# Kernel optimization log

Hardware: AMD Instinct MI355X
Metric: run time of the kernel (lower is better)

The kernel has to match this reference:

```python
import jax, jax.numpy as jnp
import numpy as np

THRESH = 0.3
PARTS = 6
D = 256
NHEAD = 8
DHEAD = 32
FF = 512
NLAYERS = 2
NUM_CLASSES = 396
EPS = 1e-5


def setup_inputs() -> dict:
    key = jax.random.key(0)
    ks = jax.random.split(key, 40)
    k = iter(ks)
    B, Q = 64, 300
    inp = {}
    inp["pred_logits"] = jax.random.normal(next(k), (B, Q, PARTS), jnp.float32)
    inp["hs"] = jax.random.normal(next(k), (B, Q, D), jnp.float32)
    for i, s in enumerate([96, 48, 24, 12]):
        inp[f"feat{i}"] = jax.random.normal(next(k), (B, D, s, s), jnp.float32)
    sc = 0.05
    inp["img_proj_w"] = sc * jax.random.normal(next(k), (4, D, D), jnp.float32)
    inp["img_proj_b"] = sc * jax.random.normal(next(k), (4, D), jnp.float32)
    inp["in_proj_w"] = sc * jax.random.normal(next(k), (NLAYERS, 3 * D, D), jnp.float32)
    inp["in_proj_b"] = sc * jax.random.normal(next(k), (NLAYERS, 3 * D), jnp.float32)
    inp["out_proj_w"] = sc * jax.random.normal(next(k), (NLAYERS, D, D), jnp.float32)
    inp["out_proj_b"] = sc * jax.random.normal(next(k), (NLAYERS, D), jnp.float32)
    inp["lin1_w"] = sc * jax.random.normal(next(k), (NLAYERS, FF, D), jnp.float32)
    inp["lin1_b"] = sc * jax.random.normal(next(k), (NLAYERS, FF), jnp.float32)
    inp["lin2_w"] = sc * jax.random.normal(next(k), (NLAYERS, D, FF), jnp.float32)
    inp["lin2_b"] = sc * jax.random.normal(next(k), (NLAYERS, D), jnp.float32)
    inp["ln1_w"] = jnp.ones((NLAYERS, D), jnp.float32)
    inp["ln1_b"] = jnp.zeros((NLAYERS, D), jnp.float32)
    inp["ln2_w"] = jnp.ones((NLAYERS, D), jnp.float32)
    inp["ln2_b"] = jnp.zeros((NLAYERS, D), jnp.float32)
    inp["cls1_w"] = sc * jax.random.normal(next(k), (512, D), jnp.float32)
    inp["cls1_b"] = sc * jax.random.normal(next(k), (512,), jnp.float32)
    inp["cls2_w"] = sc * jax.random.normal(next(k), (NUM_CLASSES, 512), jnp.float32)
    inp["cls2_b"] = sc * jax.random.normal(next(k), (NUM_CLASSES,), jnp.float32)
    return inp


def _layer_norm(x, w, b):
    m = jnp.mean(x, -1, keepdims=True)
    v = jnp.var(x, -1, keepdims=True)
    return (x - m) / jnp.sqrt(v + EPS) * w + b


def _forward(pred_logits, hs, feat0, feat1, feat2, feat3,
             img_proj_w, img_proj_b,
             in_proj_w, in_proj_b, out_proj_w, out_proj_b,
             lin1_w, lin1_b, lin2_w, lin2_b,
             ln1_w, ln1_b, ln2_w, ln2_b,
             cls1_w, cls1_b, cls2_w, cls2_b):
    B = hs.shape[0]
    # --- per-class masked mean pooling over queries (vectorized segment-mean) ---
    pred = jax.nn.sigmoid(pred_logits)                       # [B,Q,P]
    cmask = (pred > THRESH).astype(hs.dtype)                 # [B,Q,P]
    counts = cmask.sum(1)                                    # [B,P]
    csum = jnp.einsum("bqp,bqd->bpd", cmask, hs)             # [B,P,D]
    cmean = csum / jnp.maximum(counts, 1.0)[..., None]
    valid_c = counts > 0                                     # [B,P] bool
    any_valid = valid_c.any(1)                               # [B]
    # fallback: batches with no active class use hs[b, :1] in slot 0
    slot0 = jnp.where(any_valid[:, None], cmean[:, 0], hs[:, 0])
    cmean = cmean.at[:, 0].set(slot0)
    valid_c = valid_c.at[:, 0].set(valid_c[:, 0] | ~any_valid)
    # --- image tokens: global average pool + per-scale linear proj ---
    img_toks = jnp.stack([
        feat.mean((2, 3)) @ img_proj_w[i].T + img_proj_b[i]
        for i, feat in enumerate([feat0, feat1, feat2, feat3])
    ], axis=1)                                               # [B,4,D]
    tokens = jnp.concatenate([cmean, img_toks], 1)           # [B,L,D], L=PARTS+4
    valid = jnp.concatenate(
        [valid_c, jnp.ones((B, 4), bool)], 1)                # [B,L]
    NEG = jnp.asarray(-1e30, tokens.dtype)
    bias = jnp.where(valid, 0.0, NEG)[:, None, None, :]      # [B,1,1,L] key padding
    L = tokens.shape[1]
    x = tokens
    # --- 2-layer post-norm transformer encoder (eval mode, no dropout) ---
    for l in range(NLAYERS):
        qkv = x @ in_proj_w[l].T + in_proj_b[l]
        q, k_, v = jnp.split(qkv, 3, -1)
        q = q.reshape(B, L, NHEAD, DHEAD)
        k_ = k_.reshape(B, L, NHEAD, DHEAD)
        v = v.reshape(B, L, NHEAD, DHEAD)
        scores = jnp.einsum("bqhd,bkhd->bhqk", q, k_) / np.sqrt(DHEAD).astype(np.float32)
        attn = jax.nn.softmax(scores + bias, -1)
        ao = jnp.einsum("bhqk,bkhd->bqhd", attn, v).reshape(B, L, D)
        ao = ao @ out_proj_w[l].T + out_proj_b[l]
        x = _layer_norm(x + ao, ln1_w[l], ln1_b[l])
        ff = jax.nn.relu(x @ lin1_w[l].T + lin1_b[l]) @ lin2_w[l].T + lin2_b[l]
        x = _layer_norm(x + ff, ln2_w[l], ln2_b[l])
    # --- masked mean pool over valid tokens + classifier ---
    vf = valid.astype(x.dtype)
    lengths = jnp.maximum(vf.sum(1, keepdims=True), 1.0)
    cls_tok = (x * vf[..., None]).sum(1) / lengths           # [B,D]
    h = jax.nn.relu(cls_tok @ cls1_w.T + cls1_b)
    logits = h @ cls2_w.T + cls2_b                           # [B,NUM_CLASSES]
    return logits


def reference(pred_logits, hs, feat0, feat1, feat2, feat3,
              img_proj_w, img_proj_b,
              in_proj_w, in_proj_b, out_proj_w, out_proj_b,
              lin1_w, lin1_b, lin2_w, lin2_b,
              ln1_w, ln1_b, ln2_w, ln2_b,
              cls1_w, cls1_b, cls2_w, cls2_b):
    return _forward(pred_logits, hs, feat0, feat1, feat2, feat3,
                    img_proj_w, img_proj_b,
                    in_proj_w, in_proj_b, out_proj_w, out_proj_b,
                    lin1_w, lin1_b, lin2_w, lin2_b,
                    ln1_w, ln1_b, ln2_w, ln2_b,
                    cls1_w, cls1_b, cls2_w, cls2_b)
```

## Files before the change

kernel.cpp:

```cpp
#include <hip/hip_runtime.h>
#include <hip/hip_fp16.h>
#include <math.h>

#define NB 64
#define NQ 300
#define NP 6
#define ND 256
#define NF 512
#define NCL 396
#define NT 10

#define IPW_OFF 0
#define INW_OFF 262144
#define OW_OFF  655360
#define L1W_OFF 786432
#define L2W_OFF 1048576
#define C1W_OFF 1310720
#define C2W_OFF 1441792
#define TOTW    1644544
#define CONV_BLOCKS 803
#define POOL_ROWS 65536

typedef float f4 __attribute__((ext_vector_type(4)));

__device__ __forceinline__ float wred(float s) {
    #pragma unroll
    for (int o = 32; o; o >>= 1) s += __shfl_down(s, o, 64);
    return s;
}

__device__ __forceinline__ float dot8h(f4 wv, f4 xlo, f4 xhi) {
    const __half2* hp = reinterpret_cast<const __half2*>(&wv);
    float2 p0 = __half22float2(hp[0]);
    float2 p1 = __half22float2(hp[1]);
    float2 p2 = __half22float2(hp[2]);
    float2 p3 = __half22float2(hp[3]);
    return p0.x * xlo.x + p0.y * xlo.y + p1.x * xlo.z + p1.y * xlo.w
         + p2.x * xhi.x + p2.y * xhi.y + p3.x * xhi.z + p3.y * xhi.w;
}

__device__ __forceinline__ void qsync(int* flag, int tid) {
    __syncthreads();
    if (tid == 0) {
        __threadfence();
        __hip_atomic_fetch_add(flag, 1, __ATOMIC_ACQ_REL, __HIP_MEMORY_SCOPE_AGENT);
        while (__hip_atomic_load(flag, __ATOMIC_ACQUIRE, __HIP_MEMORY_SCOPE_AGENT) < 4)
            __builtin_amdgcn_s_sleep(2);
    }
    __syncthreads();
}

__global__ __launch_bounds__(256) void pool_cls_kernel(
    const float* __restrict__ pred, const float* __restrict__ hs,
    const float* __restrict__ f0, const float* __restrict__ f1,
    const float* __restrict__ f2, const float* __restrict__ f3,
    const float* __restrict__ ipw, const float* __restrict__ inw,
    const float* __restrict__ ow, const float* __restrict__ l1w,
    const float* __restrict__ l2w, const float* __restrict__ c1w,
    const float* __restrict__ c2w,
    float* __restrict__ pooled, float* __restrict__ tokG,
    float* __restrict__ biasW, __half* __restrict__ wH,
    int* __restrict__ flagW)
{
    const int bid = blockIdx.x;
    const int tid = threadIdx.x;
    __shared__ float shm[1824];

    if (bid < NB) {
        const int b = bid;
        if (tid < 16) flagW[b * 16 + tid] = 0;
        float* maskL = shm;
        float* countsL = shm + 1800;
        for (int i = tid; i < NQ * NP; i += 256) {
            float x = pred[(size_t)b * NQ * NP + i];
            float sg = 1.f / (1.f + expf(-x));
            maskL[i] = (sg > 0.3f) ? 1.f : 0.f;
        }
        __syncthreads();
        if (tid < NP) {
            float c = 0.f;
            for (int q = 0; q < NQ; q++) c += maskL[q * NP + tid];
            countsL[tid] = c;
        }
        __syncthreads();
        float acc[NP] = {0.f, 0.f, 0.f, 0.f, 0.f, 0.f};
        const float* hsb = hs + (size_t)b * NQ * ND + tid;
        for (int q = 0; q < NQ; q++) {
            float h = hsb[(size_t)q * ND];
            #pragma unroll
            for (int p = 0; p < NP; p++) acc[p] += maskL[q * NP + p] * h;
        }
        bool anyv = false;
        #pragma unroll
        for (int p = 0; p < NP; p++) anyv = anyv || (countsL[p] > 0.f);
        #pragma unroll
        for (int p = 0; p < NP; p++) {
            float cm = acc[p] / fmaxf(countsL[p], 1.f);
            if (p == 0 && !anyv) cm = hs[(size_t)b * NQ * ND + tid];
            tokG[(size_t)b * 2560 + p * ND + tid] = cm;
        }
        if (tid < 16) {
            float bv = 0.f;
            if (tid < NP) {
                bool v = countsL[tid] > 0.f;
                if (tid == 0 && !anyv) v = true;
                bv = v ? 0.f : -1e30f;
            }
            biasW[b * 16 + tid] = bv;
        }
        return;
    }

    if (bid >= NB + POOL_ROWS) {
        const int cid = bid - (NB + POOL_ROWS);
        size_t base = (size_t)cid * 2048 + (size_t)tid * 8;
        const float* src; size_t off;
        if      (base < INW_OFF) { src = ipw; off = IPW_OFF; }
        else if (base < OW_OFF)  { src = inw; off = INW_OFF; }
        else if (base < L1W_OFF) { src = ow;  off = OW_OFF;  }
        else if (base < L2W_OFF) { src = l1w; off = L1W_OFF; }
        else if (base < C1W_OFF) { src = l2w; off = L2W_OFF; }
        else if (base < C2W_OFF) { src = c1w; off = C1W_OFF; }
        else                     { src = c2w; off = C2W_OFF; }
        const f4* s4 = reinterpret_cast<const f4*>(src + (base - off));
        f4 a = s4[0], b2 = s4[1];
        union { __half2 h[4]; f4 v; } u;
        u.h[0] = __floats2half2_rn(a.x, a.y);
        u.h[1] = __floats2half2_rn(a.z, a.w);
        u.h[2] = __floats2half2_rn(b2.x, b2.y);
        u.h[3] = __floats2half2_rn(b2.z, b2.w);
        *reinterpret_cast<f4*>(wH + base) = u.v;
        return;
    }

    const int row = bid - NB;
    const int scale = row >> 14;
    const int rr = row & 16383;
    const int b = rr >> 8;
    const int d = rr & 255;
    const float* src;
    int n;
    switch (scale) {
        case 0: src = f0; n = 96 * 96; break;
        case 1: src = f1; n = 48 * 48; break;
        case 2: src = f2; n = 24 * 24; break;
        default: src = f3; n = 12 * 12; break;
    }
    const f4* p4 = reinterpret_cast<const f4*>(src + ((size_t)b * ND + d) * (size_t)n);
    int n4 = n >> 2;
    float s = 0.f;
    for (int i = tid; i < n4; i += 256) {
        f4 v = __builtin_nontemporal_load(&p4[i]);
        s += v.x + v.y + v.z + v.w;
    }
    s = wred(s);
    int wid = tid >> 6, lane = tid & 63;
    if (lane == 0) shm[wid] = s;
    __syncthreads();
    if (tid == 0) {
        float t = shm[0] + shm[1] + shm[2] + shm[3];
        pooled[((size_t)b * 4 + scale) * ND + d] = t / (float)n;
    }
}

__global__ __launch_bounds__(512) void xform_kernel(
    const float* __restrict__ pooled, float* tokG,
    const float* __restrict__ biasW, const __half* __restrict__ wH,
    const float* __restrict__ ipb, const float* __restrict__ inb,
    const float* __restrict__ ob, const float* __restrict__ l1b,
    const float* __restrict__ l2b,
    const float* __restrict__ n1w, const float* __restrict__ n1b,
    const float* __restrict__ n2w, const float* __restrict__ n2b,
    const float* __restrict__ c1b, const float* __restrict__ c2b,
    float* aoW, float* resW, float* h1W, float* hW,
    int* flagW, float* __restrict__ out)
{
    const int b  = blockIdx.x >> 2;
    const int qt = blockIdx.x & 3;
    const int tid = threadIdx.x;
    const int lane = tid & 63;
    const int wv = tid >> 6;
    int* flags = flagW + b * 16;

    __shared__ __align__(16) float xs[2560];
    __shared__ __align__(16) float loc[1920];
    __shared__ __align__(16) float buf[5120];
    __shared__ __align__(16) float part[5120];
    __shared__ float sc[224];
    __shared__ float stats[32];
    __shared__ float biasK[16];

    const f4* xs4 = reinterpret_cast<const f4*>(xs);
    const f4* buf4 = reinterpret_cast<const f4*>(buf);

    for (int i = tid; i < 1536; i += 512) xs[i] = tokG[(size_t)b * 2560 + i];
    for (int i = tid; i < 1024; i += 512) buf[i] = pooled[(size_t)b * 1024 + i];
    if (tid < 16) biasK[tid] = biasW[b * 16 + tid];
    __syncthreads();

    if (tid < 256) {
        const int i = tid >> 6, cl = tid & 63;
        const int c = qt * 64 + cl;
        const f4* w4 = reinterpret_cast<const f4*>(wH + IPW_OFF + ((size_t)(i * 256 + c)) * 256);
        float acc = 0.f;
        #pragma unroll 4
        for (int k8 = 0; k8 < 32; k8++)
            acc += dot8h(w4[k8], buf4[i * 64 + 2 * k8], buf4[i * 64 + 2 * k8 + 1]);
        tokG[(size_t)b * 2560 + (6 + i) * 256 + c] = acc + ipb[i * 256 + c];
    }
    qsync(&flags[0], tid);
    for (int i = tid + 1536; i < 2560; i += 512) xs[i] = tokG[(size_t)b * 2560 + i];
    __syncthreads();

    for (int l = 0; l < 2; l++) {
        if (tid < 384) {
            const int ks = tid / 192, cl = tid % 192;
            const int m = cl >> 6;
            const int gc = m * 256 + qt * 64 + (cl & 63);
            const f4* w4 = reinterpret_cast<const f4*>(wH + INW_OFF + ((size_t)l * 768 + gc) * 256 + ks * 128);
            float acc[NT];
            #pragma unroll
            for (int r = 0; r < NT; r++) acc[r] = 0.f;
            for (int k8 = 0; k8 < 16; k8++) {
                f4 wv4 = w4[k8];
                const int xi = ks * 32 + 2 * k8;
                #pragma unroll
                for (int r = 0; r < NT; r++)
                    acc[r] += dot8h(wv4, xs4[r * 64 + xi], xs4[r * 64 + xi + 1]);
            }
            #pragma unroll
            for (int r = 0; r < NT; r++) part[ks * 1920 + r * 192 + cl] = acc[r];
        }
        __syncthreads();
        for (int i = tid; i < 1920; i += 512) {
            int r = i / 192, cl = i - r * 192;
            int m = cl >> 6, gc = m * 256 + qt * 64 + (cl & 63);
            loc[i] = part[i] + part[1920 + i] + inb[l * 768 + gc];
        }
        __syncthreads();

        if (tid < 200) {
            int hl = tid / 100, rem = tid - 100 * hl;
            int qr = rem / 10, kr = rem - 10 * qr;
            const float* qp = &loc[qr * 192 + hl * 32];
            const float* kp = &loc[kr * 192 + 64 + hl * 32];
            float s = 0.f;
            #pragma unroll
            for (int d = 0; d < 32; d++) s += qp[d] * kp[d];
            sc[tid] = s * 0.17677669529663687f + biasK[kr];
        }
        __syncthreads();
        if (tid < 20) {
            float* row = &sc[tid * 10];
            float m = row[0];
            #pragma unroll
            for (int k = 1; k < 10; k++) m = fmaxf(m, row[k]);
            float ss = 0.f;
            #pragma unroll
            for (int k = 0; k < 10; k++) { float e = expf(row[k] - m); row[k] = e; ss += e; }
            float inv = 1.f / ss;
            #pragma unroll
            for (int k = 0; k < 10; k++) row[k] *= inv;
        }
        __syncthreads();

        for (int idx = tid; idx < 640; idx += 512) {
            int hl = idx / 320, rem = idx - 320 * hl;
            int r = rem >> 5, c = rem & 31;
            float s = 0.f;
            #pragma unroll
            for (int kr = 0; kr < 10; kr++)
                s += sc[hl * 100 + r * 10 + kr] * loc[kr * 192 + 128 + hl * 32 + c];
            aoW[(size_t)b * 2560 + r * 256 + qt * 64 + hl * 32 + c] = s;
        }
        qsync(&flags[1 + l * 4], tid);
        for (int i = tid; i < 2560; i += 512) buf[i] = aoW[(size_t)b * 2560 + i];
        __syncthreads();

        if (tid < 256) {
            const int ks = tid >> 6, cl = tid & 63;
            const int gc = qt * 64 + cl;
            const f4* w4 = reinterpret_cast<const f4*>(wH + OW_OFF + ((size_t)l * 256 + gc) * 256 + ks * 64);
            float acc[NT];
            #pragma unroll
            for (int r = 0; r < NT; r++) acc[r] = 0.f;
            for (int k8 = 0; k8 < 8; k8++) {
                f4 wv4 = w4[k8];
                const int xi = ks * 16 + 2 * k8;
                #pragma unroll
                for (int r = 0; r < NT; r++)
                    acc[r] += dot8h(wv4, buf4[r * 64 + xi], buf4[r * 64 + xi + 1]);
            }
            #pragma unroll
            for (int r = 0; r < NT; r++) part[ks * 640 + r * 64 + cl] = acc[r];
        }
        __syncthreads();
        for (int i = tid; i < 640; i += 512) {
            int r = i >> 6, cl = i & 63, gc = qt * 64 + cl;
            float v = part[i] + part[640 + i] + part[1280 + i] + part[1920 + i]
                    + ob[l * 256 + gc] + xs[r * 256 + gc];
            resW[(size_t)b * 2560 + r * 256 + gc] = v;
        }
        qsync(&flags[2 + l * 4], tid);
        for (int i = tid; i < 2560; i += 512) buf[i] = resW[(size_t)b * 2560 + i];
        __syncthreads();

        for (int r = wv; r < NT; r += 8) {
            float v0 = buf[r * 256 + lane], v1 = buf[r * 256 + 64 + lane];
            float v2 = buf[r * 256 + 128 + lane], v3 = buf[r * 256 + 192 + lane];
            float s = wred(v0 + v1 + v2 + v3);
            float q = wred(v0 * v0 + v1 * v1 + v2 * v2 + v3 * v3);
            if (lane == 0) {
                float m = s * (1.f / 256.f);
                stats[r] = m;
                stats[16 + r] = rsqrtf(fmaxf(q * (1.f / 256.f) - m * m, 0.f) + 1e-5f);
            }
        }
        __syncthreads();
        for (int i = tid; i < 2560; i += 512) {
            int r = i >> 8, c = i & 255;
            xs[i] = (buf[i] - stats[r]) * stats[16 + r] * n1w[l * 256 + c] + n1b[l * 256 + c];
        }
        __syncthreads();

        {
            const int ks = tid >> 7, cl = tid & 127;
            const int gc = qt * 128 + cl;
            const f4* w4 = reinterpret_cast<const f4*>(wH + L1W_OFF + ((size_t)l * 512 + gc) * 256 + ks * 64);
            float acc[NT];
            #pragma unroll
            for (int r = 0; r < NT; r++) acc[r] = 0.f;
            for (int k8 = 0; k8 < 8; k8++) {
                f4 wv4 = w4[k8];
                const int xi = ks * 16 + 2 * k8;
                #pragma unroll
                for (int r = 0; r < NT; r++)
                    acc[r] += dot8h(wv4, xs4[r * 64 + xi], xs4[r * 64 + xi + 1]);
            }
            __syncthreads();
            #pragma unroll
            for (int r = 0; r < NT; r++) buf[ks * 1280 + r * 128 + cl] = acc[r];
        }
        __syncthreads();
        for (int i = tid; i < 1280; i += 512) {
            int r = i >> 7, cl = i & 127, gc = qt * 128 + cl;
            float h = fmaxf(buf[i] + buf[1280 + i] + buf[2560 + i] + buf[3840 + i]
                          + l1b[l * 512 + gc], 0.f);
            h1W[(size_t)b * 5120 + r * 512 + gc] = h;
        }
        qsync(&flags[3 + l * 4], tid);
        for (int i = tid; i < 5120; i += 512) buf[i] = h1W[(size_t)b * 5120 + i];
        __syncthreads();

        {
            const int ks = tid >> 6, cl = tid & 63;
            const int gc = qt * 64 + cl;
            const f4* w4 = reinterpret_cast<const f4*>(wH + L2W_OFF + ((size_t)l * 256 + gc) * 512 + ks * 64);
            float acc[NT];
            #pragma unroll
            for (int r = 0; r < NT; r++) acc[r] = 0.f;
            for (int k8 = 0; k8 < 8; k8++) {
                f4 wv4 = w4[k8];
                const int xi = ks * 16 + 2 * k8;
                #pragma unroll
                for (int r = 0; r < NT; r++)
                    acc[r] += dot8h(wv4, buf4[r * 128 + xi], buf4[r * 128 + xi + 1]);
            }
            #pragma unroll
            for (int r = 0; r < NT; r++) part[ks * 640 + r * 64 + cl] = acc[r];
        }
        __syncthreads();
        for (int i = tid; i < 640; i += 512) {
            int r = i >> 6, cl = i & 63, gc = qt * 64 + cl;
            float v = part[i] + part[640 + i] + part[1280 + i] + part[1920 + i]
                    + part[2560 + i] + part[3200 + i] + part[3840 + i] + part[4480 + i]
                    + l2b[l * 256 + gc] + xs[r * 256 + gc];
            resW[(size_t)b * 2560 + r * 256 + gc] = v;
        }
        qsync(&flags[4 + l * 4], tid);
        for (int i = tid; i < 2560; i += 512) buf[i] = resW[(size_t)b * 2560 + i];
        __syncthreads();

        for (int r = wv; r < NT; r += 8) {
            float v0 = buf[r * 256 + lane], v1 = buf[r * 256 + 64 + lane];
            float v2 = buf[r * 256 + 128 + lane], v3 = buf[r * 256 + 192 + lane];
            float s = wred(v0 + v1 + v2 + v3);
            float q = wred(v0 * v0 + v1 * v1 + v2 * v2 + v3 * v3);
            if (lane == 0) {
                float m = s * (1.f / 256.f);
                stats[r] = m;
                stats[16 + r] = rsqrtf(fmaxf(q * (1.f / 256.f) - m * m, 0.f) + 1e-5f);
            }
        }
        __syncthreads();
        for (int i = tid; i < 2560; i += 512) {
            int r = i >> 8, c = i & 255;
            xs[i] = (buf[i] - stats[r]) * stats[16 + r] * n2w[l * 256 + c] + n2b[l * 256 + c];
        }
        __syncthreads();
    }

    if (tid < 256) {
        float len = 0.f, s = 0.f;
        #pragma unroll
        for (int r = 0; r < NT; r++) {
            float v = (biasK[r] == 0.f) ? 1.f : 0.f;
            len += v;
            s += v * xs[r * 256 + tid];
        }
        buf[tid] = s / fmaxf(len, 1.f);
    }
    __syncthreads();

    if (tid < 256) {
        const int ks = tid >> 7, cl = tid & 127;
        const int gc = qt * 128 + cl;
        const f4* w4 = reinterpret_cast<const f4*>(wH + C1W_OFF + (size_t)gc * 256 + ks * 128);
        float acc = 0.f;
        #pragma unroll 4
        for (int k8 = 0; k8 < 16; k8++)
            acc += dot8h(w4[k8], buf4[ks * 32 + 2 * k8], buf4[ks * 32 + 2 * k8 + 1]);
        part[ks * 128 + cl] = acc;
    }
    __syncthreads();
    if (tid < 128) {
        const int gc = qt * 128 + tid;
        hW[(size_t)b * 512 + gc] = fmaxf(part[tid] + part[128 + tid] + c1b[gc], 0.f);
    }
    qsync(&flags[9], tid);
    for (int i = tid; i < 512; i += 512) buf[i] = hW[(size_t)b * 512 + i];
    __syncthreads();

    if (tid < 99) {
        const int o = qt * 99 + tid;
        const f4* w4 = reinterpret_cast<const f4*>(wH + C2W_OFF + (size_t)o * 512);
        float acc = 0.f;
        #pragma unroll 4
        for (int k8 = 0; k8 < 64; k8++)
            acc += dot8h(w4[k8], buf4[2 * k8], buf4[2 * k8 + 1]);
        out[(size_t)b * NCL + o] = acc + c2b[o];
    }
}

extern "C" void kernel_launch(void* const* d_in, const int* in_sizes, int n_in,
                              void* d_out, int out_size, void* d_ws, size_t ws_size,
                              hipStream_t stream)
{
    const float* pred = (const float*)d_in[0];
    const float* hs   = (const float*)d_in[1];
    const float* f0   = (const float*)d_in[2];
    const float* f1   = (const float*)d_in[3];
    const float* f2   = (const float*)d_in[4];
    const float* f3   = (const float*)d_in[5];
    const float* ipw  = (const float*)d_in[6];
    const float* ipb  = (const float*)d_in[7];
    const float* inw  = (const float*)d_in[8];
    const float* inb  = (const float*)d_in[9];
    const float* ow   = (const float*)d_in[10];
    const float* ob   = (const float*)d_in[11];
    const float* l1w  = (const float*)d_in[12];
    const float* l1b  = (const float*)d_in[13];
    const float* l2w  = (const float*)d_in[14];
    const float* l2b  = (const float*)d_in[15];
    const float* ln1w = (const float*)d_in[16];
    const float* ln1b = (const float*)d_in[17];
    const float* ln2w = (const float*)d_in[18];
    const float* ln2b = (const float*)d_in[19];
    const float* c1w  = (const float*)d_in[20];
    const float* c1b  = (const float*)d_in[21];
    const float* c2w  = (const float*)d_in[22];
    const float* c2b  = (const float*)d_in[23];

    float* ws = (float*)d_ws;
    float* pooled = ws;
    float* tokG   = pooled + NB * 4 * ND;
    float* biasW  = tokG + NB * 2560;
    __half* wH    = (__half*)(biasW + 1024);
    float* aoW    = (float*)(wH + TOTW);
    float* resW   = aoW + NB * 2560;
    float* h1W    = resW + NB * 2560;
    float* hW     = h1W + NB * 5120;
    int*   flagW  = (int*)(hW + NB * 512);

    pool_cls_kernel<<<NB + POOL_ROWS + CONV_BLOCKS, 256, 0, stream>>>(
        pred, hs, f0, f1, f2, f3, ipw, inw, ow, l1w, l2w, c1w, c2w,
        pooled, tokG, biasW, wH, flagW);
    xform_kernel<<<4 * NB, 512, 0, stream>>>(
        pooled, tokG, biasW, wH, ipb, inb, ob, l1b, l2b,
        ln1w, ln1b, ln2w, ln2b, c1b, c2b,
        aoW, resW, h1W, hW, flagW, (float*)d_out);
}
```

Baseline: 345.3 us.

## Split matmuls by K across the four blocks per batch to cut inter-block syncs

Each of the four cooperating blocks per batch now computes partial sums over its own K-slice for the out-proj and FFN-2 matmuls. It writes full-width partials to global memory, and every block reduces all four after a single flag sync. This removes the separate all-gathers of the attention output and FFN hidden activations, cutting the per-layer qsync count from four to two. Batch/quarter indexing in blockIdx is swapped so the four blocks of one batch are spread across the grid. The cost is larger global partial buffers and redundant four-way reduction reads in every block.

```diff
diff --git a/kernel.cpp b/kernel.cpp
--- a/kernel.cpp
+++ b/kernel.cpp
@@ -172,11 +172,11 @@
     const float* __restrict__ n1w, const float* __restrict__ n1b,
     const float* __restrict__ n2w, const float* __restrict__ n2b,
     const float* __restrict__ c1b, const float* __restrict__ c2b,
-    float* aoW, float* resW, float* h1W, float* hW,
+    float* opW, float* f2W, float* hW,
     int* flagW, float* __restrict__ out)
 {
-    const int b  = blockIdx.x >> 2;
-    const int qt = blockIdx.x & 3;
+    const int b  = blockIdx.x & 63;
+    const int qt = blockIdx.x >> 6;
     const int tid = threadIdx.x;
     const int lane = tid & 63;
     const int wv = tid >> 6;
@@ -184,17 +184,19 @@
 
     __shared__ __align__(16) float xs[2560];
     __shared__ __align__(16) float loc[1920];
-    __shared__ __align__(16) float buf[5120];
-    __shared__ __align__(16) float part[5120];
+    __shared__ __align__(16) float res[2560];
+    __shared__ __align__(16) float h1a[1280];
+    __shared__ __align__(16) float pp[3840];
     __shared__ float sc[224];
     __shared__ float stats[32];
     __shared__ float biasK[16];
 
     const f4* xs4 = reinterpret_cast<const f4*>(xs);
-    const f4* buf4 = reinterpret_cast<const f4*>(buf);
-
-    for (int i = tid; i < 1536; i += 512) xs[i] = tokG[(size_t)b * 2560 + i];
-    for (int i = tid; i < 1024; i += 512) buf[i] = pooled[(size_t)b * 1024 + i];
+    const f4* loc4 = reinterpret_cast<const f4*>(loc);
+    const f4* res4 = reinterpret_cast<const f4*>(res);
+    const f4* h1a4 = reinterpret_cast<const f4*>(h1a);
+
+    for (int i = tid; i < 1024; i += 512) loc[i] = pooled[(size_t)b * 1024 + i];
     if (tid < 16) biasK[tid] = biasW[b * 16 + tid];
     __syncthreads();
 
@@ -205,11 +207,11 @@
         float acc = 0.f;
         #pragma unroll 4
         for (int k8 = 0; k8 < 32; k8++)
-            acc += dot8h(w4[k8], buf4[i * 64 + 2 * k8], buf4[i * 64 + 2 * k8 + 1]);
+            acc += dot8h(w4[k8], loc4[i * 64 + 2 * k8], loc4[i * 64 + 2 * k8 + 1]);
         tokG[(size_t)b * 2560 + (6 + i) * 256 + c] = acc + ipb[i * 256 + c];
     }
     qsync(&flags[0], tid);
-    for (int i = tid + 1536; i < 2560; i += 512) xs[i] = tokG[(size_t)b * 2560 + i];
+    for (int i = tid; i < 2560; i += 512) xs[i] = tokG[(size_t)b * 2560 + i];
     __syncthreads();
 
     for (int l = 0; l < 2; l++) {
@@ -229,13 +231,13 @@
                     acc[r] += dot8h(wv4, xs4[r * 64 + xi], xs4[r * 64 + xi + 1]);
             }
             #pragma unroll
-            for (int r = 0; r < NT; r++) part[ks * 1920 + r * 192 + cl] = acc[r];
+            for (int r = 0; r < NT; r++) pp[ks * 1920 + r * 192 + cl] = acc[r];
         }
         __syncthreads();
         for (int i = tid; i < 1920; i += 512) {
             int r = i / 192, cl = i - r * 192;
             int m = cl >> 6, gc = m * 256 + qt * 64 + (cl & 63);
-            loc[i] = part[i] + part[1920 + i] + inb[l * 768 + gc];
+            loc[i] = pp[i] + pp[1920 + i] + inb[l * 768 + gc];
         }
         __syncthreads();
 
@@ -271,43 +273,40 @@
             #pragma unroll
             for (int kr = 0; kr < 10; kr++)
                 s += sc[hl * 100 + r * 10 + kr] * loc[kr * 192 + 128 + hl * 32 + c];
-            aoW[(size_t)b * 2560 + r * 256 + qt * 64 + hl * 32 + c] = s;
-        }
-        qsync(&flags[1 + l * 4], tid);
-        for (int i = tid; i < 2560; i += 512) buf[i] = aoW[(size_t)b * 2560 + i];
-        __syncthreads();
-
-        if (tid < 256) {
-            const int ks = tid >> 6, cl = tid & 63;
-            const int gc = qt * 64 + cl;
-            const f4* w4 = reinterpret_cast<const f4*>(wH + OW_OFF + ((size_t)l * 256 + gc) * 256 + ks * 64);
-            float acc[NT];
-            #pragma unroll
-            for (int r = 0; r < NT; r++) acc[r] = 0.f;
+            h1a[r * 64 + hl * 32 + c] = s;
+        }
+        __syncthreads();
+
+        {
+            const int c = tid & 255, rh = tid >> 8;
+            const f4* w4 = reinterpret_cast<const f4*>(wH + OW_OFF + ((size_t)l * 256 + c) * 256 + qt * 64);
+            float acc[5];
+            #pragma unroll
+            for (int rr = 0; rr < 5; rr++) acc[rr] = 0.f;
             for (int k8 = 0; k8 < 8; k8++) {
                 f4 wv4 = w4[k8];
-                const int xi = ks * 16 + 2 * k8;
                 #pragma unroll
-                for (int r = 0; r < NT; r++)
-                    acc[r] += dot8h(wv4, buf4[r * 64 + xi], buf4[r * 64 + xi + 1]);
-            }
-            #pragma unroll
-            for (int r = 0; r < NT; r++) part[ks * 640 + r * 64 + cl] = acc[r];
-        }
-        __syncthreads();
-        for (int i = tid; i < 640; i += 512) {
-            int r = i >> 6, cl = i & 63, gc = qt * 64 + cl;
-            float v = part[i] + part[640 + i] + part[1280 + i] + part[1920 + i]
-                    + ob[l * 256 + gc] + xs[r * 256 + gc];
-            resW[(size_t)b * 2560 + r * 256 + gc] = v;
-        }
-        qsync(&flags[2 + l * 4], tid);
-        for (int i = tid; i < 2560; i += 512) buf[i] = resW[(size_t)b * 2560 + i];
-        __syncthreads();
-
+                for (int rr = 0; rr < 5; rr++) {
+                    int r = rh * 5 + rr;
+                    acc[rr] += dot8h(wv4, h1a4[r * 16 + 2 * k8], h1a4[r * 16 + 2 * k8 + 1]);
+                }
+            }
+            #pragma unroll
+            for (int rr = 0; rr < 5; rr++)
+                opW[((size_t)(b * 4 + qt)) * 2560 + (rh * 5 + rr) * 256 + c] = acc[rr];
+        }
+        qsync(&flags[1 + 2 * l], tid);
+
+        for (int i = tid; i < 2560; i += 512) {
+            float v = opW[(size_t)(b * 4 + 0) * 2560 + i] + opW[(size_t)(b * 4 + 1) * 2560 + i]
+                    + opW[(size_t)(b * 4 + 2) * 2560 + i] + opW[(size_t)(b * 4 + 3) * 2560 + i]
+                    + ob[l * 256 + (i & 255)] + xs[i];
+            res[i] = v;
+        }
+        __syncthreads();
         for (int r = wv; r < NT; r += 8) {
-            float v0 = buf[r * 256 + lane], v1 = buf[r * 256 + 64 + lane];
-            float v2 = buf[r * 256 + 128 + lane], v3 = buf[r * 256 + 192 + lane];
+            float v0 = res[r * 256 + lane], v1 = res[r * 256 + 64 + lane];
+            float v2 = res[r * 256 + 128 + lane], v3 = res[r * 256 + 192 + lane];
             float s = wred(v0 + v1 + v2 + v3);
             float q = wred(v0 * v0 + v1 * v1 + v2 * v2 + v3 * v3);
             if (lane == 0) {
@@ -319,71 +318,62 @@
         __syncthreads();
         for (int i = tid; i < 2560; i += 512) {
             int r = i >> 8, c = i & 255;
-            xs[i] = (buf[i] - stats[r]) * stats[16 + r] * n1w[l * 256 + c] + n1b[l * 256 + c];
+            xs[i] = (res[i] - stats[r]) * stats[16 + r] * n1w[l * 256 + c] + n1b[l * 256 + c];
+        }
+        __syncthreads();
+
+        if (tid < 256) {
+            const int cl = tid & 127, rh = (tid >> 7) & 1;
+            const int gc = qt * 128 + cl;
+            const f4* w4 = reinterpret_cast<const f4*>(wH + L1W_OFF + ((size_t)l * 512 + gc) * 256);
+            float acc[5];
+            #pragma unroll
+            for (int rr = 0; rr < 5; rr++) acc[rr] = 0.f;
+            for (int k8 = 0; k8 < 32; k8++) {
+                f4 wv4 = w4[k8];
+                #pragma unroll
+                for (int rr = 0; rr < 5; rr++) {
+                    int r = rh * 5 + rr;
+                    acc[rr] += dot8h(wv4, xs4[r * 64 + 2 * k8], xs4[r * 64 + 2 * k8 + 1]);
+                }
+            }
+            float bb = l1b[l * 512 + gc];
+            #pragma unroll
+            for (int rr = 0; rr < 5; rr++)
+                h1a[(rh * 5 + rr) * 128 + cl] = fmaxf(acc[rr] + bb, 0.f);
         }
         __syncthreads();
 
         {
-            const int ks = tid >> 7, cl = tid & 127;
-            const int gc = qt * 128 + cl;
-            const f4* w4 = reinterpret_cast<const f4*>(wH + L1W_OFF + ((size_t)l * 512 + gc) * 256 + ks * 64);
-            float acc[NT];
-            #pragma unroll
-            for (int r = 0; r < NT; r++) acc[r] = 0.f;
-            for (int k8 = 0; k8 < 8; k8++) {
+            const int c = tid & 255, rh = tid >> 8;
+            const f4* w4 = reinterpret_cast<const f4*>(wH + L2W_OFF + ((size_t)l * 256 + c) * 512 + qt * 128);
+            float acc[5];
+            #pragma unroll
+            for (int rr = 0; rr < 5; rr++) acc[rr] = 0.f;
+            for (int k8 = 0; k8 < 16; k8++) {
                 f4 wv4 = w4[k8];
-                const int xi = ks * 16 + 2 * k8;
                 #pragma unroll
-                for (int r = 0; r < NT; r++)
-                    acc[r] += dot8h(wv4, xs4[r * 64 + xi], xs4[r * 64 + xi + 1]);
-            }
-            __syncthreads();
-            #pragma unroll
-            for (int r = 0; r < NT; r++) buf[ks * 1280 + r * 128 + cl] = acc[r];
-        }
-        __syncthreads();
-        for (int i = tid; i < 1280; i += 512) {
-            int r = i >> 7, cl = i & 127, gc = qt * 128 + cl;
-            float h = fmaxf(buf[i] + buf[1280 + i] + buf[2560 + i] + buf[3840 + i]
-                          + l1b[l * 512 + gc], 0.f);
-            h1W[(size_t)b * 5120 + r * 512 + gc] = h;
-        }
-        qsync(&flags[3 + l * 4], tid);
-        for (int i = tid; i < 5120; i += 512) buf[i] = h1W[(size_t)b * 5120 + i];
-        __syncthreads();
-
-        {
-            const int ks = tid >> 6, cl = tid & 63;
-            const int gc = qt * 64 + cl;
-            const f4* w4 = reinterpret_cast<const f4*>(wH + L2W_OFF + ((size_t)l * 256 + gc) * 512 + ks * 64);
-            float acc[NT];
-            #pragma unroll
-            for (int r = 0; r < NT; r++) acc[r] = 0.f;
-            for (int k8 = 0; k8 < 8; k8++) {
-                f4 wv4 = w4[k8];
-                const int xi = ks * 16 + 2 * k8;
-                #pragma unroll
-                for (int r = 0; r < NT; r++)
-                    acc[r] += dot8h(wv4, buf4[r * 128 + xi], buf4[r * 128 + xi + 1]);
-            }
-            #pragma unroll
-            for (int r = 0; r < NT; r++) part[ks * 640 + r * 64 + cl] = acc[r];
-        }
-        __syncthreads();
-        for (int i = tid; i < 640; i += 512) {
-            int r = i >> 6, cl = i & 63, gc = qt * 64 + cl;
-            float v = part[i] + part[640 + i] + part[1280 + i] + part[1920 + i]
-                    + part[2560 + i] + part[3200 + i] + part[3840 + i] + part[4480 + i]
-                    + l2b[l * 256 + gc] + xs[r * 256 + gc];
-            resW[(size_t)b * 2560 + r * 256 + gc] = v;
-        }
-        qsync(&flags[4 + l * 4], tid);
-        for (int i = tid; i < 2560; i += 512) buf[i] = resW[(size_t)b * 2560 + i];
-        __syncthreads();
-
+                for (int rr = 0; rr < 5; rr++) {
+                    int r = rh * 5 + rr;
+                    acc[rr] += dot8h(wv4, h1a4[r * 32 + 2 * k8], h1a4[r * 32 + 2 * k8 + 1]);
+                }
+            }
+            #pragma unroll
+            for (int rr = 0; rr < 5; rr++)
+                f2W[((size_t)(b * 4 + qt)) * 2560 + (rh * 5 + rr) * 256 + c] = acc[rr];
+        }
+        qsync(&flags[2 + 2 * l], tid);
+
+        for (int i = tid; i < 2560; i += 512) {
+            float v = f2W[(size_t)(b * 4 + 0) * 2560 + i] + f2W[(size_t)(b * 4 + 1) * 2560 + i]
+                    + f2W[(size_t)(b * 4 + 2) * 2560 + i] + f2W[(size_t)(b * 4 + 3) * 2560 + i]
+                    + l2b[l * 256 + (i & 255)] + xs[i];
+            res[i] = v;
+        }
+        __syncthreads();
         for (int r = wv; r < NT; r += 8) {
-            float v0 = buf[r * 256 + lane], v1 = buf[r * 256 + 64 + lane];
-            float v2 = buf[r * 256 + 128 + lane], v3 = buf[r * 256 + 192 + lane];
+            float v0 = res[r * 256 + lane], v1 = res[r * 256 + 64 + lane];
+            float v2 = res[r * 256 + 128 + lane], v3 = res[r * 256 + 192 + lane];
             float s = wred(v0 + v1 + v2 + v3);
             float q = wred(v0 * v0 + v1 * v1 + v2 * v2 + v3 * v3);
             if (lane == 0) {
@@ -395,7 +385,7 @@
         __syncthreads();
         for (int i = tid; i < 2560; i += 512) {
             int r = i >> 8, c = i & 255;
-            xs[i] = (buf[i] - stats[r]) * stats[16 + r] * n2w[l * 256 + c] + n2b[l * 256 + c];
+            xs[i] = (res[i] - stats[r]) * stats[16 + r] * n2w[l * 256 + c] + n2b[l * 256 + c];
         }
         __syncthreads();
     }
@@ -408,27 +398,27 @@
             len += v;
             s += v * xs[r * 256 + tid];
         }
-        buf[tid] = s / fmaxf(len, 1.f);
+        res[tid] = s / fmaxf(len, 1.f);
     }
     __syncthreads();
 
     if (tid < 256) {
-        const int ks = tid >> 7, cl = tid & 127;
+        const int kh = tid >> 7, cl = tid & 127;
         const int gc = qt * 128 + cl;
-        const f4* w4 = reinterpret_cast<const f4*>(wH + C1W_OFF + (size_t)gc * 256 + ks * 128);
+        const f4* w4 = reinterpret_cast<const f4*>(wH + C1W_OFF + (size_t)gc * 256 + kh * 128);
         float acc = 0.f;
         #pragma unroll 4
         for (int k8 = 0; k8 < 16; k8++)
-            acc += dot8h(w4[k8], buf4[ks * 32 + 2 * k8], buf4[ks * 32 + 2 * k8 + 1]);
-        part[ks * 128 + cl] = acc;
+            acc += dot8h(w4[k8], res4[kh * 32 + 2 * k8], res4[kh * 32 + 2 * k8 + 1]);
+        pp[kh * 128 + cl] = acc;
     }
     __syncthreads();
     if (tid < 128) {
         const int gc = qt * 128 + tid;
-        hW[(size_t)b * 512 + gc] = fmaxf(part[tid] + part[128 + tid] + c1b[gc], 0.f);
-    }
-    qsync(&flags[9], tid);
-    for (int i = tid; i < 512; i += 512) buf[i] = hW[(size_t)b * 512 + i];
+        hW[(size_t)b * 512 + gc] = fmaxf(pp[tid] + pp[128 + tid] + c1b[gc], 0.f);
+    }
+    qsync(&flags[5], tid);
+    for (int i = tid; i < 512; i += 512) res[i] = hW[(size_t)b * 512 + i];
     __syncthreads();
 
     if (tid < 99) {
@@ -437,7 +427,7 @@
         float acc = 0.f;
         #pragma unroll 4
         for (int k8 = 0; k8 < 64; k8++)
-            acc += dot8h(w4[k8], buf4[2 * k8], buf4[2 * k8 + 1]);
+            acc += dot8h(w4[k8], res4[2 * k8], res4[2 * k8 + 1]);
         out[(size_t)b * NCL + o] = acc + c2b[o];
     }
 }
@@ -476,10 +466,9 @@
     float* tokG   = pooled + NB * 4 * ND;
     float* biasW  = tokG + NB * 2560;
     __half* wH    = (__half*)(biasW + 1024);
-    float* aoW    = (float*)(wH + TOTW);
-    float* resW   = aoW + NB * 2560;
-    float* h1W    = resW + NB * 2560;
-    float* hW     = h1W + NB * 5120;
+    float* opW    = (float*)(wH + TOTW);
+    float* f2W    = opW + NB * 4 * 2560;
+    float* hW     = f2W + NB * 4 * 2560;
     int*   flagW  = (int*)(hW + NB * 512);
 
     pool_cls_kernel<<<NB + POOL_ROWS + CONV_BLOCKS, 256, 0, stream>>>(
@@ -488,5 +477,5 @@
     xform_kernel<<<4 * NB, 512, 0, stream>>>(
         pooled, tokG, biasW, wH, ipb, inb, ob, l1b, l2b,
         ln1w, ln1b, ln2w, ln2b, c1b, c2b,
-        aoW, resW, h1W, hW, flagW, (float*)d_out);
-}
+        opW, f2W, hW, flagW, (float*)d_out);
+}
```

New measurement: 283.0 us. 1.22x faster.
